# Kernel optimization log

Measured on AMD Instinct MI355X. Metric: run time of the kernel, lower is better.

## Reference

```python
import jax, jax.numpy as jnp
import numpy as np

HEADS = 8

def _flatten(x, s1, s2):
    # 'b c (h s1) (w s2) -> b (h w) (s1 s2 c)'
    b, c, H, W = x.shape
    h, w = H // s1, W // s2
    x = x.reshape(b, c, h, s1, w, s2).transpose(0, 2, 4, 3, 5, 1)
    return x.reshape(b, h * w, s1 * s2 * c)

def _unflatten(x, h, w, s1, s2):
    # 'b (h w) (s1 s2 c) -> b c (h s1) (w s2)'
    b, n, e = x.shape
    c = e // (s1 * s2)
    x = x.reshape(b, h, w, s1, s2, c).transpose(0, 5, 1, 3, 2, 4)
    return x.reshape(b, c, h * s1, w * s2)

def _attn(x_detail, x_context, wq, bq, wk, bk, wv, bv, wo, bo):
    E = x_detail.shape[-1]
    d = E // HEADS
    scale = d ** -0.5
    def split(t):
        b, n, _ = t.shape
        return t.reshape(b, n, HEADS, d).transpose(0, 2, 1, 3)  # b h n d
    q = split(x_context @ wq.T + bq)
    k = split(x_detail @ wk.T + bk)
    v = split(x_detail @ wv.T + bv)
    att = jax.nn.softmax(jnp.einsum('bhqd,bhkd->bhqk', q, k) * scale, axis=-1)
    out = jnp.einsum('bhqk,bhkd->bhqd', att, v)
    b, h, n, _ = out.shape
    out = out.transpose(0, 2, 1, 3).reshape(b, n, E)
    return out @ wo.T + bo

def setup_inputs() -> dict:
    key = jax.random.key(0)
    ks = iter(jax.random.split(key, 64))
    inp = {}
    xshapes = [(16, 96, 56, 56), (16, 192, 28, 28), (16, 384, 14, 14), (16, 768, 7, 7)]
    names = ['x00', 'x10', 'x20', 'x30']
    for nm, sh in zip(names, xshapes):
        inp[nm + '_detail'] = jax.random.normal(next(ks), sh, dtype=jnp.float32)
        inp[nm + '_context'] = jax.random.normal(next(ks), sh, dtype=jnp.float32)
    embs = [384, 192, 384, 768]
    for i, E in enumerate(embs):
        for p in ['q', 'k', 'v', 'o']:
            inp[f'w{p}{i}'] = jax.random.normal(next(ks), (E, E), dtype=jnp.float32) * 0.02
            inp[f'b{p}{i}'] = jnp.zeros((E,), dtype=jnp.float32)
    return inp

def reference(x00_detail, x00_context, x10_detail, x10_context,
              x20_detail, x20_context, x30_detail, x30_context,
              wq0, bq0, wk0, bk0, wv0, bv0, wo0, bo0,
              wq1, bq1, wk1, bk1, wv1, bv1, wo1, bo1,
              wq2, bq2, wk2, bk2, wv2, bv2, wo2, bo2,
              wq3, bq3, wk3, bk3, wv3, bv3, wo3, bo3):
    # scale 0: 56x56 with 2x2 patching -> 784 tokens, emb 384
    o0 = x00_detail + _unflatten(
        _attn(_flatten(x00_detail, 2, 2), _flatten(x00_context, 2, 2),
              wq0, bq0, wk0, bk0, wv0, bv0, wo0, bo0), 28, 28, 2, 2)
    # scale 1: 28x28 -> 784 tokens, emb 192
    o1 = x10_detail + _unflatten(
        _attn(_flatten(x10_detail, 1, 1), _flatten(x10_context, 1, 1),
              wq1, bq1, wk1, bk1, wv1, bv1, wo1, bo1), 28, 28, 1, 1)
    # scale 2: 14x14 -> 196 tokens, emb 384
    o2 = x20_detail + _unflatten(
        _attn(_flatten(x20_detail, 1, 1), _flatten(x20_context, 1, 1),
              wq2, bq2, wk2, bk2, wv2, bv2, wo2, bo2), 14, 14, 1, 1)
    # scale 3: 7x7 -> 49 tokens, emb 768
    o3 = x30_detail + _unflatten(
        _attn(_flatten(x30_detail, 1, 1), _flatten(x30_context, 1, 1),
              wq3, bq3, wk3, bk3, wv3, bv3, wo3, bo3), 7, 7, 1, 1)
    return (o0, o1, o2, o3)
```

## Files before the change

### kernel.cpp

```cpp
#include <hip/hip_runtime.h>
#include <hip/hip_bf16.h>
#include <cstdint>
#include <cstddef>
#include <cmath>

typedef unsigned short bf16u;
typedef float f32x4 __attribute__((ext_vector_type(4)));
typedef short frag8 __attribute__((ext_vector_type(8)));

typedef __attribute__((address_space(1))) uint32_t u32g;
typedef __attribute__((address_space(3))) uint32_t u32l;

__device__ __forceinline__ void async_cp16(const bf16u* g, bf16u* l) {
    __builtin_amdgcn_global_load_lds((u32g*)g, (u32l*)l, 16, 0, 0);
}

__device__ __forceinline__ bf16u f2bf(float f) {
    union { float f; uint32_t u; } v; v.f = f;
    uint32_t u = v.u;
    return (bf16u)((u + 0x7fffu + ((u >> 16) & 1u)) >> 16);
}

__device__ __forceinline__ uint32_t pk2bf(float a, float b) {
    __hip_bfloat162 h = __float22bfloat162_rn(make_float2(a, b));
    union { __hip_bfloat162 h; uint32_t u; } c; c.h = h; return c.u;
}

__device__ __forceinline__ int vperm(int n) {
    return (n & ~63) | ((n & 15) << 2) | ((n >> 4) & 3);
}

static constexpr int cN[4]   = {784, 784, 196, 49};
static constexpr int cE[4]   = {384, 192, 384, 768};
static constexpr int cM[4]   = {12544, 12544, 3136, 784};
static constexpr int cC[4]   = {96, 192, 384, 768};
static constexpr int cH[4]   = {56, 28, 14, 7};
static constexpr int cS[4]   = {2, 1, 1, 1};
static constexpr int cWt[4]  = {28, 28, 14, 7};

static constexpr size_t xoff[4] = {0, 4816896, 7225344, 8429568};
static constexpr size_t voff[4] = {0, 6815744, 10223616, 12320768};
static constexpr size_t woff[4] = {0, 589824, 737280, 1327104};

__device__ __constant__ float qsc[4] = {0.20823509f, 0.29448888f, 0.20823509f, 0.14724444f};

static constexpr int qStartQ[5] = {0, 294, 369, 411, 999};
static constexpr int oStart[5]  = {0,294,369,411,999};

static constexpr int fStart[9] = {0,4800,9600,12000,14400,15744,17088,17856,18624};
static constexpr int wCum[17]  = {0,72,144,216,288,306,324,342,360,432,504,576,648,936,1224,1512,1800};
static constexpr int fNtn[4] = {25, 25, 7, 2};
static constexpr int fNtc[4] = {3, 6, 12, 24};
static constexpr int fSp[4]  = {4, 1, 1, 1};

struct BiasP { const float* p[16]; };
struct PrepP { const float* x[8]; const float* w[16]; };
struct OunfP { const float* xd[4]; };

__global__ __launch_bounds__(256) void prep(PrepP pp, bf16u* __restrict__ Xd,
                                            bf16u* __restrict__ Xc, bf16u* __restrict__ Wb) {
    int blk = blockIdx.x, tid = threadIdx.x;
    if (blk < 18624) {
        __shared__ float tile[32][33];
        int seg = 0;
        while (seg < 7 && blk >= fStart[seg + 1]) seg++;
        int s = seg >> 1, which = seg & 1;
        int l = blk - fStart[seg];
        int ntn = fNtn[s], ntc = fNtc[s], sp = fSp[s];
        int nt = l % ntn; l /= ntn;
        int ctl = l % ntc; l /= ntc;
        int spi = l % sp; int b = l / sp;
        int sv = cS[s];
        int s1i = spi / sv, s2i = spi % sv;
        int C = cC[s], H = cH[s], Wd = cH[s], N = cN[s], E2 = cE[s], Wt = cWt[s];
        const float* x = pp.x[s * 2 + which];
        bf16u* dst = (which ? Xc : Xd) + xoff[s];
        int tx = tid & 31, ty = tid >> 5;
        int n0 = nt * 32, c0 = ctl * 32;
#pragma unroll
        for (int rr = 0; rr < 4; ++rr) {
            int c = c0 + rr * 8 + ty;
            int n = n0 + tx;
            if (n < N) {
                int hh = (n / Wt) * sv + s1i;
                int ww = (n % Wt) * sv + s2i;
                tile[rr * 8 + ty][tx] = x[((size_t)(b * C + c) * H + hh) * Wd + ww];
            }
        }
        __syncthreads();
        int ebase = (s1i * sv + s2i) * C + c0;
#pragma unroll
        for (int rr = 0; rr < 4; ++rr) {
            int n = n0 + rr * 8 + ty;
            if (n < N)
                dst[((size_t)b * N + n) * E2 + ebase + tx] = f2bf(tile[tx][rr * 8 + ty]);
        }
    } else {
        int wb = blk - 18624;
        int m2 = 0;
        while (m2 < 15 && wb >= wCum[m2 + 1]) m2++;
        int s = m2 >> 2, mi = m2 & 3;
        size_t e2 = (size_t)cE[s] * cE[s];
        size_t base = (size_t)(wb - wCum[m2]) * 2048 + tid * 8;
        const float* src = pp.w[m2];
        bf16u* dst = Wb + woff[s] + mi * e2 + base;
        float4 a = *(const float4*)(src + base);
        float4 c = *(const float4*)(src + base + 4);
        bf16u o[8] = {f2bf(a.x), f2bf(a.y), f2bf(a.z), f2bf(a.w),
                      f2bf(c.x), f2bf(c.y), f2bf(c.z), f2bf(c.w)};
        *(frag8*)dst = *(frag8*)o;
    }
}

template<int MODE, int NN, int DHt, int DHPt, int NJt>
__device__ __forceinline__ void gemm_tile128(const bf16u* __restrict__ A, const bf16u* __restrict__ W,
                                             const float* __restrict__ bias,
                                             int M, int E, int mTile, int eTile, float oscale,
                                             bf16u* __restrict__ outB,
                                             bf16u* sm) {
    bf16u* A0 = sm;
    bf16u* B0 = sm + 4096;
    bf16u* A1 = sm + 8192;
    bf16u* B1 = sm + 12288;
    int tid = threadIdx.x, wave = tid >> 6, lane = tid & 63;
    int mbase = mTile * 128, ebase = eTile * 128;
    int wm = (wave & 1) * 64, wn = (wave >> 1) * 64;
    f32x4 acc[4][4] = {};
    int srow = tid >> 2, sch = (tid & 3) * 8;
    int K = E;
    int m0 = mbase + srow;      if (m0 >= M) m0 = M - 1;
    int m1 = mbase + srow + 64; if (m1 >= M) m1 = M - 1;
    const bf16u* Ag0 = A + (size_t)m0 * K + sch;
    const bf16u* Ag1 = A + (size_t)m1 * K + sch;
    const bf16u* Wg0 = W + (size_t)(ebase + srow) * K + sch;
    const bf16u* Wg1 = W + (size_t)(ebase + srow + 64) * K + sch;
    int la = (lane & 15) * 32 + (lane >> 4) * 8;

    auto stage = [&](int k0, bf16u* As, bf16u* Bs) {
        async_cp16(Ag0 + k0, As + tid * 8);
        async_cp16(Ag1 + k0, As + 2048 + tid * 8);
        async_cp16(Wg0 + k0, Bs + tid * 8);
        async_cp16(Wg1 + k0, Bs + 2048 + tid * 8);
    };
    auto compute = [&](const bf16u* As, const bf16u* Bs) {
        frag8 af[4], bfr[4];
#pragma unroll
        for (int i = 0; i < 4; ++i) {
            af[i]  = *(const frag8*)(As + (wm + i * 16) * 32 + la);
            bfr[i] = *(const frag8*)(Bs + (wn + i * 16) * 32 + la);
        }
#pragma unroll
        for (int i = 0; i < 4; ++i)
#pragma unroll
            for (int j = 0; j < 4; ++j)
                acc[i][j] = __builtin_amdgcn_mfma_f32_16x16x32_bf16(af[i], bfr[j], acc[i][j], 0, 0, 0);
    };

    stage(0, A0, B0);
    __syncthreads();
    for (int k0 = 0; k0 < K; k0 += 64) {
        stage(k0 + 32, A1, B1);
        compute(A0, B0);
        __syncthreads();
        if (k0 + 64 < K) stage(k0 + 64, A0, B0);
        compute(A1, B1);
        if (k0 + 64 < K) __syncthreads();
    }

#pragma unroll
    for (int mt = 0; mt < 4; ++mt) {
#pragma unroll
        for (int nt = 0; nt < 4; ++nt) {
            int col = ebase + wn + nt * 16 + (lane & 15);
            float bv = bias[col];
            int rbase = mbase + wm + mt * 16 + (lane >> 4) * 4;
#pragma unroll
            for (int r = 0; r < 4; ++r) {
                int rowg = rbase + r;
                if (rowg >= M) continue;
                float val = (acc[mt][nt][r] + bv) * oscale;
                if (MODE == 0) {
                    outB[(size_t)rowg * E + col] = f2bf(val);
                } else {
                    int bb2 = rowg / NN, n = rowg % NN;
                    int hh = col / DHt, d = col - hh * DHt;
                    outB[((size_t)(bb2 * 8 + hh) * DHPt + d) * NJt + vperm(n)] = f2bf(val);
                }
            }
        }
    }
}

template<int MODE, int NN, int DHt, int DHPt, int NJt>
__device__ __forceinline__ void gemm_tile64(const bf16u* __restrict__ A, const bf16u* __restrict__ W,
                                            const float* __restrict__ bias,
                                            int M, int E, int mTile, int eTile, float oscale,
                                            bf16u* __restrict__ outB,
                                            bf16u* sm) {
    bf16u* A0 = sm;
    bf16u* B0 = sm + 2048;
    bf16u* A1 = sm + 4096;
    bf16u* B1 = sm + 6144;
    int tid = threadIdx.x, wave = tid >> 6, lane = tid & 63;
    int mbase = mTile * 64, ebase = eTile * 64;
    int wm = (wave & 1) * 32, wn = (wave >> 1) * 32;
    f32x4 acc[2][2] = {};
    int srow = tid >> 2, sch = (tid & 3) * 8;
    int K = E;
    int m = mbase + srow; if (m >= M) m = M - 1;
    const bf16u* Ag = A + (size_t)m * K + sch;
    const bf16u* Wg = W + (size_t)(ebase + srow) * K + sch;
    int la = (lane & 15) * 32 + (lane >> 4) * 8;

    auto stage = [&](int k0, bf16u* As, bf16u* Bs) {
        async_cp16(Ag + k0, As + tid * 8);
        async_cp16(Wg + k0, Bs + tid * 8);
    };
    auto compute = [&](const bf16u* As, const bf16u* Bs) {
        frag8 af0 = *(const frag8*)(As + wm * 32 + la);
        frag8 af1 = *(const frag8*)(As + (wm + 16) * 32 + la);
        frag8 bf0 = *(const frag8*)(Bs + wn * 32 + la);
        frag8 bf1 = *(const frag8*)(Bs + (wn + 16) * 32 + la);
        acc[0][0] = __builtin_amdgcn_mfma_f32_16x16x32_bf16(af0, bf0, acc[0][0], 0, 0, 0);
        acc[0][1] = __builtin_amdgcn_mfma_f32_16x16x32_bf16(af0, bf1, acc[0][1], 0, 0, 0);
        acc[1][0] = __builtin_amdgcn_mfma_f32_16x16x32_bf16(af1, bf0, acc[1][0], 0, 0, 0);
        acc[1][1] = __builtin_amdgcn_mfma_f32_16x16x32_bf16(af1, bf1, acc[1][1], 0, 0, 0);
    };

    stage(0, A0, B0);
    __syncthreads();
    for (int k0 = 0; k0 < K; k0 += 64) {
        stage(k0 + 32, A1, B1);
        compute(A0, B0);
        __syncthreads();
        if (k0 + 64 < K) stage(k0 + 64, A0, B0);
        compute(A1, B1);
        if (k0 + 64 < K) __syncthreads();
    }

#pragma unroll
    for (int mt = 0; mt < 2; ++mt) {
#pragma unroll
        for (int nt = 0; nt < 2; ++nt) {
            int col = ebase + wn + nt * 16 + (lane & 15);
            float bv = bias[col];
            int rbase = mbase + wm + mt * 16 + (lane >> 4) * 4;
#pragma unroll
            for (int r = 0; r < 4; ++r) {
                int rowg = rbase + r;
                if (rowg >= M) continue;
                float val = (acc[mt][nt][r] + bv) * oscale;
                if (MODE == 0) {
                    outB[(size_t)rowg * E + col] = f2bf(val);
                } else {
                    int bb2 = rowg / NN, n = rowg % NN;
                    int hh = col / DHt, d = col - hh * DHt;
                    outB[((size_t)(bb2 * 8 + hh) * DHPt + d) * NJt + vperm(n)] = f2bf(val);
                }
            }
        }
    }
}

template<int NN, int DHt, int DHPt, int NJt>
__device__ __forceinline__ void gemm_kv128(const bf16u* __restrict__ A, const bf16u* __restrict__ Wk,
                                           const bf16u* __restrict__ Wv,
                                           const float* __restrict__ bk, const float* __restrict__ bv,
                                           int M, int E, int mTile, int eTile,
                                           bf16u* __restrict__ Ko, bf16u* __restrict__ Vo, bf16u* sm) {
    bf16u* A0 = sm;           bf16u* K0 = sm + 4096;   bf16u* V0 = sm + 8192;
    bf16u* A1 = sm + 12288;   bf16u* K1 = sm + 16384;  bf16u* V1 = sm + 20480;
    int tid = threadIdx.x, wave = tid >> 6, lane = tid & 63;
    int mbase = mTile * 128, ebase = eTile * 128;
    int wm = (wave & 1) * 64, wn = (wave >> 1) * 64;
    f32x4 acck[4][4] = {};
    f32x4 accv[4][4] = {};
    int srow = tid >> 2, sch = (tid & 3) * 8;
    int Kd = E;
    int m0 = mbase + srow;      if (m0 >= M) m0 = M - 1;
    int m1 = mbase + srow + 64; if (m1 >= M) m1 = M - 1;
    const bf16u* Ag0 = A + (size_t)m0 * Kd + sch;
    const bf16u* Ag1 = A + (size_t)m1 * Kd + sch;
    const bf16u* Kg0 = Wk + (size_t)(ebase + srow) * Kd + sch;
    const bf16u* Kg1 = Wk + (size_t)(ebase + srow + 64) * Kd + sch;
    const bf16u* Vg0 = Wv + (size_t)(ebase + srow) * Kd + sch;
    const bf16u* Vg1 = Wv + (size_t)(ebase + srow + 64) * Kd + sch;
    int la = (lane & 15) * 32 + (lane >> 4) * 8;

    auto stage = [&](int k0, bf16u* As, bf16u* Ks, bf16u* Vs) {
        async_cp16(Ag0 + k0, As + tid * 8);
        async_cp16(Ag1 + k0, As + 2048 + tid * 8);
        async_cp16(Kg0 + k0, Ks + tid * 8);
        async_cp16(Kg1 + k0, Ks + 2048 + tid * 8);
        async_cp16(Vg0 + k0, Vs + tid * 8);
        async_cp16(Vg1 + k0, Vs + 2048 + tid * 8);
    };
    auto compute = [&](const bf16u* As, const bf16u* Ks, const bf16u* Vs) {
        frag8 af[4], bfr[4];
#pragma unroll
        for (int i = 0; i < 4; ++i)
            af[i] = *(const frag8*)(As + (wm + i * 16) * 32 + la);
#pragma unroll
        for (int i = 0; i < 4; ++i)
            bfr[i] = *(const frag8*)(Ks + (wn + i * 16) * 32 + la);
#pragma unroll
        for (int i = 0; i < 4; ++i)
#pragma unroll
            for (int j = 0; j < 4; ++j)
                acck[i][j] = __builtin_amdgcn_mfma_f32_16x16x32_bf16(af[i], bfr[j], acck[i][j], 0, 0, 0);
#pragma unroll
        for (int i = 0; i < 4; ++i)
            bfr[i] = *(const frag8*)(Vs + (wn + i * 16) * 32 + la);
#pragma unroll
        for (int i = 0; i < 4; ++i)
#pragma unroll
            for (int j = 0; j < 4; ++j)
                accv[i][j] = __builtin_amdgcn_mfma_f32_16x16x32_bf16(af[i], bfr[j], accv[i][j], 0, 0, 0);
    };

    stage(0, A0, K0, V0);
    __syncthreads();
    for (int k0 = 0; k0 < Kd; k0 += 64) {
        stage(k0 + 32, A1, K1, V1);
        compute(A0, K0, V0);
        __syncthreads();
        if (k0 + 64 < Kd) stage(k0 + 64, A0, K0, V0);
        compute(A1, K1, V1);
        if (k0 + 64 < Kd) __syncthreads();
    }

#pragma unroll
    for (int mt = 0; mt < 4; ++mt) {
#pragma unroll
        for (int nt = 0; nt < 4; ++nt) {
            int col = ebase + wn + nt * 16 + (lane & 15);
            float bkc = bk[col];
            float bvc = bv[col];
            int hh = col / DHt, d = col - hh * DHt;
            int rbase = mbase + wm + mt * 16 + (lane >> 4) * 4;
#pragma unroll
            for (int r = 0; r < 4; ++r) {
                int rowg = rbase + r;
                if (rowg >= M) continue;
                Ko[(size_t)rowg * E + col] = f2bf(acck[mt][nt][r] + bkc);
                int bb2 = rowg / NN, n = rowg % NN;
                Vo[((size_t)(bb2 * 8 + hh) * DHPt + d) * NJt + vperm(n)] = f2bf(accv[mt][nt][r] + bvc);
            }
        }
    }
}

template<int NN, int DHt, int DHPt, int NJt>
__device__ __forceinline__ void gemm_kv64(const bf16u* __restrict__ A, const bf16u* __restrict__ Wk,
                                          const bf16u* __restrict__ Wv,
                                          const float* __restrict__ bk, const float* __restrict__ bv,
                                          int M, int E, int mTile, int eTile,
                                          bf16u* __restrict__ Ko, bf16u* __restrict__ Vo, bf16u* sm) {
    bf16u* A0 = sm;          bf16u* K0 = sm + 2048;  bf16u* V0 = sm + 4096;
    bf16u* A1 = sm + 6144;   bf16u* K1 = sm + 8192;  bf16u* V1 = sm + 10240;
    int tid = threadIdx.x, wave = tid >> 6, lane = tid & 63;
    int mbase = mTile * 64, ebase = eTile * 64;
    int wm = (wave & 1) * 32, wn = (wave >> 1) * 32;
    f32x4 acck[2][2] = {};
    f32x4 accv[2][2] = {};
    int srow = tid >> 2, sch = (tid & 3) * 8;
    int Kd = E;
    int m = mbase + srow; if (m >= M) m = M - 1;
    const bf16u* Ag = A + (size_t)m * Kd + sch;
    const bf16u* Kg = Wk + (size_t)(ebase + srow) * Kd + sch;
    const bf16u* Vg = Wv + (size_t)(ebase + srow) * Kd + sch;
    int la = (lane & 15) * 32 + (lane >> 4) * 8;

    auto stage = [&](int k0, bf16u* As, bf16u* Ks, bf16u* Vs) {
        async_cp16(Ag + k0, As + tid * 8);
        async_cp16(Kg + k0, Ks + tid * 8);
        async_cp16(Vg + k0, Vs + tid * 8);
    };
    auto compute = [&](const bf16u* As, const bf16u* Ks, const bf16u* Vs) {
        frag8 af0 = *(const frag8*)(As + wm * 32 + la);
        frag8 af1 = *(const frag8*)(As + (wm + 16) * 32 + la);
        frag8 k0f = *(const frag8*)(Ks + wn * 32 + la);
        frag8 k1f = *(const frag8*)(Ks + (wn + 16) * 32 + la);
        acck[0][0] = __builtin_amdgcn_mfma_f32_16x16x32_bf16(af0, k0f, acck[0][0], 0, 0, 0);
        acck[0][1] = __builtin_amdgcn_mfma_f32_16x16x32_bf16(af0, k1f, acck[0][1], 0, 0, 0);
        acck[1][0] = __builtin_amdgcn_mfma_f32_16x16x32_bf16(af1, k0f, acck[1][0], 0, 0, 0);
        acck[1][1] = __builtin_amdgcn_mfma_f32_16x16x32_bf16(af1, k1f, acck[1][1], 0, 0, 0);
        frag8 v0f = *(const frag8*)(Vs + wn * 32 + la);
        frag8 v1f = *(const frag8*)(Vs + (wn + 16) * 32 + la);
        accv[0][0] = __builtin_amdgcn_mfma_f32_16x16x32_bf16(af0, v0f, accv[0][0], 0, 0, 0);
        accv[0][1] = __builtin_amdgcn_mfma_f32_16x16x32_bf16(af0, v1f, accv[0][1], 0, 0, 0);
        accv[1][0] = __builtin_amdgcn_mfma_f32_16x16x32_bf16(af1, v0f, accv[1][0], 0, 0, 0);
        accv[1][1] = __builtin_amdgcn_mfma_f32_16x16x32_bf16(af1, v1f, accv[1][1], 0, 0, 0);
    };

    stage(0, A0, K0, V0);
    __syncthreads();
    for (int k0 = 0; k0 < Kd; k0 += 64) {
        stage(k0 + 32, A1, K1, V1);
        compute(A0, K0, V0);
        __syncthreads();
        if (k0 + 64 < Kd) stage(k0 + 64, A0, K0, V0);
        compute(A1, K1, V1);
        if (k0 + 64 < Kd) __syncthreads();
    }

#pragma unroll
    for (int mt = 0; mt < 2; ++mt) {
#pragma unroll
        for (int nt = 0; nt < 2; ++nt) {
            int col = ebase + wn + nt * 16 + (lane & 15);
            float bkc = bk[col];
            float bvc = bv[col];
            int hh = col / DHt, d = col - hh * DHt;
            int rbase = mbase + wm + mt * 16 + (lane >> 4) * 4;
#pragma unroll
            for (int r = 0; r < 4; ++r) {
                int rowg = rbase + r;
                if (rowg >= M) continue;
                Ko[(size_t)rowg * E + col] = f2bf(acck[mt][nt][r] + bkc);
                int bb2 = rowg / NN, n = rowg % NN;
                Vo[((size_t)(bb2 * 8 + hh) * DHPt + d) * NJt + vperm(n)] = f2bf(accv[mt][nt][r] + bvc);
            }
        }
    }
}

__global__ __launch_bounds__(256) void qkv_q(const bf16u* __restrict__ Xc, const bf16u* __restrict__ Wb,
                                             bf16u* __restrict__ Qb, BiasP bp) {
    __shared__ __align__(16) bf16u sm[16384];
    int blk = blockIdx.x;
    int seg = 0;
    while (seg < 3 && blk >= qStartQ[seg + 1]) seg++;
    int t = blk - qStartQ[seg];
    if (seg < 3) {
        int s = (seg == 0) ? 0 : (seg == 1 ? 2 : 3);
        int E = cE[s], M = cM[s];
        int ct = E >> 7;
        int mTile = t / ct, eTile = t - mTile * ct;
        gemm_tile128<0, 0, 1, 0, 0>(Xc + xoff[s], Wb + woff[s], bp.p[s * 4], M, E, mTile, eTile,
                                    qsc[s], Qb + xoff[s], sm);
    } else {
        int E = 192, M = 12544;
        int mTile = t / 3, eTile = t - mTile * 3;
        gemm_tile64<0, 0, 1, 0, 0>(Xc + xoff[1], Wb + woff[1], bp.p[4], M, E, mTile, eTile,
                                   qsc[1], Qb + xoff[1], sm);
    }
}

__global__ __launch_bounds__(256, 2) void qkv_kv(const bf16u* __restrict__ Xd, const bf16u* __restrict__ Wb,
                                                 bf16u* __restrict__ Kb, bf16u* __restrict__ Vt, BiasP bp) {
    __shared__ __align__(16) bf16u sm[24576];
    int blk = blockIdx.x;
    int seg = 0;
    while (seg < 3 && blk >= qStartQ[seg + 1]) seg++;
    int t = blk - qStartQ[seg];
    if (seg < 3) {
        int s = (seg == 0) ? 0 : (seg == 1 ? 2 : 3);
        int E = cE[s], M = cM[s];
        int ct = E >> 7;
        int mTile = t / ct, eTile = t - mTile * ct;
        const bf16u* A  = Xd + xoff[s];
        const bf16u* Wk = Wb + woff[s] + (size_t)1 * E * E;
        const bf16u* Wv = Wb + woff[s] + (size_t)2 * E * E;
        if (s == 0)
            gemm_kv128<784, 48, 64, 832>(A, Wk, Wv, bp.p[1], bp.p[2], M, E, mTile, eTile,
                                         Kb + xoff[0], Vt + voff[0], sm);
        else if (s == 2)
            gemm_kv128<196, 48, 64, 256>(A, Wk, Wv, bp.p[9], bp.p[10], M, E, mTile, eTile,
                                         Kb + xoff[2], Vt + voff[2], sm);
        else
            gemm_kv128<49, 96, 96, 64>(A, Wk, Wv, bp.p[13], bp.p[14], M, E, mTile, eTile,
                                       Kb + xoff[3], Vt + voff[3], sm);
    } else {
        int E = 192, M = 12544;
        int mTile = t / 3, eTile = t - mTile * 3;
        gemm_kv64<784, 24, 32, 832>(Xd + xoff[1], Wb + woff[1] + (size_t)1 * E * E,
                                    Wb + woff[1] + (size_t)2 * E * E, bp.p[5], bp.p[6],
                                    M, E, mTile, eTile, Kb + xoff[1], Vt + voff[1], sm);
    }
}

__device__ __forceinline__ f32x4 bfly_add16(f32x4 v) {
#pragma unroll
    for (int m = 1; m <= 8; m <<= 1) {
        f32x4 o;
#pragma unroll
        for (int e = 0; e < 4; ++e) o[e] = __shfl_xor(v[e], m);
#pragma unroll
        for (int e = 0; e < 4; ++e) v[e] += o[e];
    }
    return v;
}

template<int DH, int N>
__device__ __forceinline__ void attn_body2(bf16u* __restrict__ smem,
                                           const bf16u* __restrict__ Q, const bf16u* __restrict__ K,
                                           const bf16u* __restrict__ Vt, bf16u* __restrict__ O,
                                           int lin) {
    constexpr int DHP = (DH == 24) ? 32 : 64;
    constexpr int C8  = DHP / 8;
    constexpr int CM  = C8 - 1;
    constexpr int KC  = DHP / 32;
    constexpr int DHT = (DH + 15) / 16;
    constexpr int VR  = DHT * 16;
    constexpr int NT  = (N + 63) / 64;
    constexpr int NJc = NT * 64;
    constexpr int E   = DH * 8;
    constexpr int KS  = 64 * C8;
    constexpr int TS  = KS + VR * 8;
    constexpr int RND = (TS + 255) / 256;
    constexpr int PP  = 72;

    bf16u* buf0 = smem;
    bf16u* buf1 = smem + (size_t)TS * 8;
    bf16u* Ps   = smem + (size_t)2 * TS * 8;

    const int qt = lin % NT;
    const int r2 = lin / NT;
    const int h = r2 & 7, b = r2 >> 3;
    const int qb = qt * 64;
    const int tid = threadIdx.x, wave = tid >> 6, lane = tid & 63;
    const int mrow = lane & 15, quad = lane >> 4;

    const bf16u* Kb2 = K + (size_t)b * N * E + h * DH;
    const bf16u* Vb2 = Vt + (size_t)(b * 8 + h) * DHP * NJc;

    auto stage = [&](int jt, bf16u* buf) {
#pragma unroll
        for (int r = 0; r < RND; ++r) {
            int s = tid + r * 256;
            bf16u* dst = buf + (size_t)s * 8;
            if (s < KS) {
                int row = s / C8;
                int cl = (s & CM) ^ (row & CM);
                int n = jt * 64 + row; if (n >= N) n = N - 1;
                async_cp16(Kb2 + (size_t)n * E + cl * 8, dst);
            } else if (s < TS) {
                int v = s - KS;
                int d = v >> 3;
                int cl = (v & 7) ^ (d & 7);
                async_cp16(Vb2 + (size_t)d * NJc + jt * 64 + cl * 8, dst);
            }
        }
    };

    stage(0, buf0);

    frag8 qf[KC];
    {
        int qn = qb + wave * 16 + mrow; if (qn >= N) qn = N - 1;
        const bf16u* qp = Q + (size_t)(b * N + qn) * E + h * DH;
#pragma unroll
        for (int kc = 0; kc < KC; ++kc) {
            int col = kc * 32 + quad * 8;
            frag8 v = {};
            if (col < DH) v = *(const frag8*)(qp + col);
            qf[kc] = v;
        }
    }

    f32x4 lrun = {0.f, 0.f, 0.f, 0.f};
    f32x4 oacc[DHT];
#pragma unroll
    for (int t = 0; t < DHT; ++t) oacc[t] = f32x4{0.f, 0.f, 0.f, 0.f};

    bf16u* Pw = Ps + wave * 16 * PP;

    __syncthreads();

    int p = 0;
    for (int jt = 0; jt < NT; ++jt) {
        bf16u* KsB = p ? buf1 : buf0;
        bf16u* VsB = KsB + (size_t)KS * 8;
        if (jt + 1 < NT) stage(jt + 1, p ? buf0 : buf1);

        f32x4 s[4];
        const bool domask = ((N & 63) != 0) && (jt == NT - 1);
#pragma unroll
        for (int sub = 0; sub < 4; ++sub) {
            f32x4 acc = {};
#pragma unroll
            for (int kc = 0; kc < KC; ++kc) {
                int c = kc * 4 + quad;
                frag8 bfr = *(const frag8*)(KsB + ((size_t)((sub * 16 + mrow) * C8 + (c ^ (mrow & CM)))) * 8);
                acc = __builtin_amdgcn_mfma_f32_16x16x32_bf16(qf[kc], bfr, acc, 0, 0, 0);
            }
            if (domask) {
                int col = jt * 64 + sub * 16 + mrow;
                if (col >= N) { acc[0] = acc[1] = acc[2] = acc[3] = -30000.f; }
            }
            s[sub] = acc;
        }

#pragma unroll
        for (int sub = 0; sub < 4; ++sub)
#pragma unroll
            for (int e = 0; e < 4; ++e) {
                float px = __builtin_amdgcn_exp2f(s[sub][e]);
                s[sub][e] = px;
                lrun[e] += px;
            }

#pragma unroll
        for (int e = 0; e < 4; ++e) {
            uint2 u;
            u.x = pk2bf(s[0][e], s[1][e]);
            u.y = pk2bf(s[2][e], s[3][e]);
            *(uint2*)(Pw + (quad * 4 + e) * PP + mrow * 4) = u;
        }

#pragma unroll
        for (int jc = 0; jc < 2; ++jc) {
            frag8 af = *(const frag8*)(Pw + mrow * PP + jc * 32 + quad * 8);
            int c = jc * 4 + quad;
#pragma unroll
            for (int t = 0; t < DHT; ++t) {
                frag8 bfr = *(const frag8*)(VsB + ((size_t)((t * 16 + mrow) * 8 + (c ^ (mrow & 7)))) * 8);
                oacc[t] = __builtin_amdgcn_mfma_f32_16x16x32_bf16(af, bfr, oacc[t], 0, 0, 0);
            }
        }
        __syncthreads();
        p ^= 1;
    }

    lrun = bfly_add16(lrun);
    f32x4 linv;
#pragma unroll
    for (int e = 0; e < 4; ++e) linv[e] = 1.0f / lrun[e];
#pragma unroll
    for (int t = 0; t < DHT; ++t) {
        int d = t * 16 + mrow;
        if (d >= DH) continue;
#pragma unroll
        for (int e = 0; e < 4; ++e) {
            int n = qb + wave * 16 + quad * 4 + e;
            if (n < N)
                O[((size_t)(b * N + n)) * E + h * DH + d] = f2bf(oacc[t][e] * linv[e]);
        }
    }
}

__global__ __launch_bounds__(256, 4) void attn_fat(const bf16u* __restrict__ Qb, const bf16u* __restrict__ Kb,
                                                   const bf16u* __restrict__ Vt, bf16u* __restrict__ Ob) {
    __shared__ __align__(16) bf16u smem[18944];
    int g = blockIdx.x;
    if (g < 1664) {
        int l = (g & 7) * 208 + (g >> 3);
        attn_body2<48, 784>(smem, Qb + xoff[0], Kb + xoff[0], Vt + voff[0], Ob + xoff[0], l);
    } else if (g < 3328) {
        int gg = g - 1664;
        int l = (gg & 7) * 208 + (gg >> 3);
        attn_body2<24, 784>(smem, Qb + xoff[1], Kb + xoff[1], Vt + voff[1], Ob + xoff[1], l);
    } else {
        int gg = g - 3328;
        int l = (gg & 7) * 64 + (gg >> 3);
        attn_body2<48, 196>(smem, Qb + xoff[2], Kb + xoff[2], Vt + voff[2], Ob + xoff[2], l);
    }
}

__global__ __launch_bounds__(256, 2) void attn_s3(const bf16u* __restrict__ Qg, const bf16u* __restrict__ Kg,
                                                  const bf16u* __restrict__ Vtg, bf16u* __restrict__ Og) {
    constexpr int DH = 96, N = 49, DHP = 96, KC = 3, DHT = 6, NJc = 64, E = 768;
    constexpr int KP = 104, QP = 104, VP = 72, PP = 72, C8 = 12;
    __shared__ __align__(16) bf16u smem[20224];
    bf16u* Ks = smem;
    bf16u* Vs = Ks + 64 * KP;
    bf16u* QsPw = Vs + DHT * 16 * VP;

    const bf16u* Q = Qg + xoff[3];
    const bf16u* K = Kg + xoff[3];
    const bf16u* Vt = Vtg + voff[3];
    bf16u* O = Og + xoff[3];

    int lin = blockIdx.x;
    int h = lin & 7, b = lin >> 3;
    int tid = threadIdx.x, wave = tid >> 6, lane = tid & 63;
    int mrow = lane & 15, quad = lane >> 4;

    for (int idx = tid; idx < 64 * C8; idx += 256) {
        int row = idx / C8, col = (idx % C8) * 8;
        int n = row; if (n >= N) n = N - 1;
        frag8 v = {};
        if (col < DH) v = *(const frag8*)(Q + ((size_t)(b * N + n)) * E + h * DH + col);
        *(frag8*)(QsPw + row * QP + col) = v;
    }
    for (int idx = tid; idx < 64 * C8; idx += 256) {
        int row = idx / C8, col = (idx % C8) * 8;
        int n = row; if (n >= N) n = N - 1;
        frag8 v = {};
        if (col < DH) v = *(const frag8*)(K + (size_t)(b * N + n) * E + h * DH + col);
        *(frag8*)(Ks + row * KP + col) = v;
    }
    const bf16u* Vb2 = Vt + (size_t)(b * 8 + h) * DHP * NJc;
    for (int idx = tid; idx < DHT * 16 * 8; idx += 256) {
        int d = idx / 8, j = (idx % 8) * 8;
        frag8 v = {};
        if (d < DH) v = *(const frag8*)(Vb2 + (size_t)d * NJc + j);
        *(frag8*)(Vs + d * VP + j) = v;
    }
    __syncthreads();
    frag8 qf[KC];
#pragma unroll
    for (int kc = 0; kc < KC; ++kc)
        qf[kc] = *(const frag8*)(QsPw + (wave * 16 + mrow) * QP + kc * 32 + quad * 8);
    __syncthreads();
    bf16u* Pw = QsPw + wave * 16 * PP;

    f32x4 lrun = {0.f, 0.f, 0.f, 0.f};
    f32x4 oacc[DHT];
#pragma unroll
    for (int t = 0; t < DHT; ++t) oacc[t] = f32x4{0.f, 0.f, 0.f, 0.f};

    f32x4 s[4];
#pragma unroll
    for (int sub = 0; sub < 4; ++sub) {
        f32x4 acc = {};
#pragma unroll
        for (int kc = 0; kc < KC; ++kc) {
            frag8 bfr = *(const frag8*)(Ks + (sub * 16 + mrow) * KP + kc * 32 + quad * 8);
            acc = __builtin_amdgcn_mfma_f32_16x16x32_bf16(qf[kc], bfr, acc, 0, 0, 0);
        }
        int col = sub * 16 + mrow;
        if (col >= N) { acc[0] = acc[1] = acc[2] = acc[3] = -30000.f; }
        s[sub] = acc;
    }
#pragma unroll
    for (int sub = 0; sub < 4; ++sub)
#pragma unroll
        for (int e = 0; e < 4; ++e) {
            float px = __builtin_amdgcn_exp2f(s[sub][e]);
            s[sub][e] = px;
            lrun[e] += px;
        }
#pragma unroll
    for (int e = 0; e < 4; ++e) {
        uint2 u;
        u.x = pk2bf(s[0][e], s[1][e]);
        u.y = pk2bf(s[2][e], s[3][e]);
        *(uint2*)(Pw + (quad * 4 + e) * PP + mrow * 4) = u;
    }
#pragma unroll
    for (int jc = 0; jc < 2; ++jc) {
        frag8 af = *(const frag8*)(Pw + mrow * PP + jc * 32 + quad * 8);
#pragma unroll
        for (int t = 0; t < DHT; ++t) {
            frag8 bfr = *(const frag8*)(Vs + (t * 16 + mrow) * VP + jc * 32 + quad * 8);
            oacc[t] = __builtin_amdgcn_mfma_f32_16x16x32_bf16(af, bfr, oacc[t], 0, 0, 0);
        }
    }

    lrun = bfly_add16(lrun);
    f32x4 linv;
#pragma unroll
    for (int e = 0; e < 4; ++e) linv[e] = 1.0f / lrun[e];
#pragma unroll
    for (int t = 0; t < DHT; ++t) {
        int d = t * 16 + mrow;
#pragma unroll
        for (int e = 0; e < 4; ++e) {
            int n = wave * 16 + quad * 4 + e;
            if (n < N)
                O[((size_t)(b * N + n)) * E + h * DH + d] = f2bf(oacc[t][e] * linv[e]);
        }
    }
}

template<int SC>
__device__ __forceinline__ size_t out_index(int rowg, int cg) {
    if (SC == 0) {
        int b = rowg / 784, n = rowg - b * 784;
        int slot = cg / 96, c = cg - slot * 96;
        int hh = n / 28, ww = n - hh * 28;
        return ((size_t)(b * 96 + c) * 56 + 2 * hh + (slot >> 1)) * 56 + 2 * ww + (slot & 1);
    } else if (SC == 1) {
        int b = rowg / 784, n = rowg - b * 784;
        return ((size_t)(b * 192 + cg)) * 784 + n;
    } else if (SC == 2) {
        int b = rowg / 196, n = rowg - b * 196;
        return ((size_t)(b * 384 + cg)) * 196 + n;
    } else {
        int b = rowg / 49, n = rowg - b * 49;
        return ((size_t)(b * 768 + cg)) * 49 + n;
    }
}

template<int SC>
__device__ __forceinline__ void o_tile128(const bf16u* __restrict__ A, const bf16u* __restrict__ W,
                                          const float* __restrict__ bias,
                                          const float* __restrict__ xd, float* __restrict__ out,
                                          int M, int E, int mTile, int eTile, bf16u* sm) {
    bf16u* A0 = sm;
    bf16u* B0 = sm + 4096;
    bf16u* A1 = sm + 8192;
    bf16u* B1 = sm + 12288;
    int tid = threadIdx.x, wave = tid >> 6, lane = tid & 63;
    int mbase = mTile * 128, ebase = eTile * 128;
    int wm = (wave & 1) * 64, wn = (wave >> 1) * 64;
    int mrow = lane & 15, quad = lane >> 4;
    f32x4 acc[4][4] = {};
    int srow = tid >> 2, sch = (tid & 3) * 8;
    int K = E;
    int m0 = mbase + srow;      if (m0 >= M) m0 = M - 1;
    int m1 = mbase + srow + 64; if (m1 >= M) m1 = M - 1;
    const bf16u* Ag0 = A + (size_t)m0 * K + sch;
    const bf16u* Ag1 = A + (size_t)m1 * K + sch;
    const bf16u* Wg0 = W + (size_t)(ebase + srow) * K + sch;
    const bf16u* Wg1 = W + (size_t)(ebase + srow + 64) * K + sch;
    int la = mrow * 32 + quad * 8;

    auto stage = [&](int k0, bf16u* As, bf16u* Bs) {
        async_cp16(Ag0 + k0, As + tid * 8);
        async_cp16(Ag1 + k0, As + 2048 + tid * 8);
        async_cp16(Wg0 + k0, Bs + tid * 8);
        async_cp16(Wg1 + k0, Bs + 2048 + tid * 8);
    };
    auto compute = [&](const bf16u* As, const bf16u* Bs) {
        frag8 af[4], bfr[4];
#pragma unroll
        for (int i = 0; i < 4; ++i) {
            af[i]  = *(const frag8*)(As + (wm + i * 16) * 32 + la);
            bfr[i] = *(const frag8*)(Bs + (wn + i * 16) * 32 + la);
        }
#pragma unroll
        for (int i = 0; i < 4; ++i)
#pragma unroll
            for (int j = 0; j < 4; ++j)
                acc[i][j] = __builtin_amdgcn_mfma_f32_16x16x32_bf16(af[i], bfr[j], acc[i][j], 0, 0, 0);
    };

    stage(0, A0, B0);
    __syncthreads();
    for (int k0 = 0; k0 < K; k0 += 64) {
        stage(k0 + 32, A1, B1);
        compute(A0, B0);
        __syncthreads();
        if (k0 + 64 < K) stage(k0 + 64, A0, B0);
        compute(A1, B1);
        if (k0 + 64 < K) __syncthreads();
    }

    float* Ls = (float*)sm;
#pragma unroll
    for (int ph = 0; ph < 4; ++ph) {
        __syncthreads();
        if ((wave & 1) == (ph >> 1)) {
            int mt0 = (ph & 1) * 2;
#pragma unroll
            for (int mi = 0; mi < 2; ++mi) {
                int mt = mt0 + mi;
#pragma unroll
                for (int nt = 0; nt < 4; ++nt)
#pragma unroll
                    for (int r = 0; r < 4; ++r)
                        Ls[(mi * 16 + quad * 4 + r) * 133 + wn + nt * 16 + mrow] = acc[mt][nt][r];
            }
        }
        __syncthreads();
        int rb = mbase + ph * 32;
#pragma unroll
        for (int i = 0; i < 16; ++i) {
            int coll = (tid >> 5) + i * 8;
            int l = tid & 31;
            int rg = rb + l;
            if (rg < M) {
                int cg = ebase + coll;
                size_t oi = out_index<SC>(rg, cg);
                out[oi] = xd[oi] + Ls[l * 133 + coll] + bias[cg];
            }
        }
    }
}

__device__ __forceinline__ void o_tile64_s1(const bf16u* __restrict__ A, const bf16u* __restrict__ W,
                                            const float* __restrict__ bias,
                                            const float* __restrict__ xd, float* __restrict__ out,
                                            int M, int E, int mTile, int eTile, bf16u* sm) {
    bf16u* A0 = sm;
    bf16u* B0 = sm + 2048;
    bf16u* A1 = sm + 4096;
    bf16u* B1 = sm + 6144;
    int tid = threadIdx.x, wave = tid >> 6, lane = tid & 63;
    int mbase = mTile * 64, ebase = eTile * 64;
    int wm = (wave & 1) * 32, wn = (wave >> 1) * 32;
    int mrow = lane & 15, quad = lane >> 4;
    f32x4 acc[2][2] = {};
    int srow = tid >> 2, sch = (tid & 3) * 8;
    int K = E;
    int m = mbase + srow; if (m >= M) m = M - 1;
    const bf16u* Ag = A + (size_t)m * K + sch;
    const bf16u* Wg = W + (size_t)(ebase + srow) * K + sch;
    int la = mrow * 32 + quad * 8;

    auto stage = [&](int k0, bf16u* As, bf16u* Bs) {
        async_cp16(Ag + k0, As + tid * 8);
        async_cp16(Wg + k0, Bs + tid * 8);
    };
    auto compute = [&](const bf16u* As, const bf16u* Bs) {
        frag8 af0 = *(const frag8*)(As + wm * 32 + la);
        frag8 af1 = *(const frag8*)(As + (wm + 16) * 32 + la);
        frag8 bf0 = *(const frag8*)(Bs + wn * 32 + la);
        frag8 bf1 = *(const frag8*)(Bs + (wn + 16) * 32 + la);
        acc[0][0] = __builtin_amdgcn_mfma_f32_16x16x32_bf16(af0, bf0, acc[0][0], 0, 0, 0);
        acc[0][1] = __builtin_amdgcn_mfma_f32_16x16x32_bf16(af0, bf1, acc[0][1], 0, 0, 0);
        acc[1][0] = __builtin_amdgcn_mfma_f32_16x16x32_bf16(af1, bf0, acc[1][0], 0, 0, 0);
        acc[1][1] = __builtin_amdgcn_mfma_f32_16x16x32_bf16(af1, bf1, acc[1][1], 0, 0, 0);
    };

    stage(0, A0, B0);
    __syncthreads();
    for (int k0 = 0; k0 < K; k0 += 64) {
        stage(k0 + 32, A1, B1);
        compute(A0, B0);
        __syncthreads();
        if (k0 + 64 < K) stage(k0 + 64, A0, B0);
        compute(A1, B1);
        if (k0 + 64 < K) __syncthreads();
    }

    float* Ls = (float*)sm;
#pragma unroll
    for (int ph = 0; ph < 2; ++ph) {
        __syncthreads();
        if ((wave & 1) == ph) {
#pragma unroll
            for (int mt = 0; mt < 2; ++mt)
#pragma unroll
                for (int nt = 0; nt < 2; ++nt)
#pragma unroll
                    for (int r = 0; r < 4; ++r)
                        Ls[(mt * 16 + quad * 4 + r) * 69 + wn + nt * 16 + mrow] = acc[mt][nt][r];
        }
        __syncthreads();
        int rb = mbase + ph * 32;
#pragma unroll
        for (int i = 0; i < 8; ++i) {
            int coll = (tid >> 5) + i * 8;
            int l = tid & 31;
            int rg = rb + l;
            if (rg < M) {
                int cg = ebase + coll;
                size_t oi = out_index<1>(rg, cg);
                out[oi] = xd[oi] + Ls[l * 69 + coll] + bias[cg];
            }
        }
    }
}

__global__ __launch_bounds__(256) void ounf_fat(const bf16u* __restrict__ Ob, const bf16u* __restrict__ Wb,
                                                float* __restrict__ out, BiasP bp, OunfP up) {
    __shared__ __align__(16) bf16u sm[16384];
    int blk = blockIdx.x;
    int seg = 0;
    while (seg < 3 && blk >= oStart[seg + 1]) seg++;
    int t = blk - oStart[seg];
    if (seg < 3) {
        int s = (seg == 0) ? 0 : (seg == 1 ? 2 : 3);
        int E = cE[s], M = cM[s];
        int ct = E >> 7;
        int mTile = t / ct, eTile = t - mTile * ct;
        const bf16u* A = Ob + xoff[s];
        const bf16u* W = Wb + woff[s] + (size_t)3 * E * E;
        if (s == 0)
            o_tile128<0>(A, W, bp.p[3], up.xd[0], out + xoff[0], M, E, mTile, eTile, sm);
        else if (s == 2)
            o_tile128<2>(A, W, bp.p[11], up.xd[2], out + xoff[2], M, E, mTile, eTile, sm);
        else
            o_tile128<3>(A, W, bp.p[15], up.xd[3], out + xoff[3], M, E, mTile, eTile, sm);
    } else {
        int E = 192, M = 12544;
        int mTile = t / 3, eTile = t - mTile * 3;
        o_tile64_s1(Ob + xoff[1], Wb + woff[1] + (size_t)3 * E * E, bp.p[7],
                    up.xd[1], out + xoff[1], M, E, mTile, eTile, sm);
    }
}

extern "C" void kernel_launch(void* const* d_in, const int* in_sizes, int n_in,
                              void* d_out, int out_size, void* d_ws, size_t ws_size,
                              hipStream_t stream) {
    bf16u* ws = (bf16u*)d_ws;
    bf16u* Qb = ws;
    bf16u* Kb = ws + 9031680;
    bf16u* Vt = ws + 18063360;
    bf16u* Ob = ws + 31170560;
    bf16u* Wb = ws + 40202240;
    bf16u* Xd = ws + 43888640;
    bf16u* Xc = ws + 52920320;
    float* out = (float*)d_out;

    PrepP pp; BiasP bb; OunfP ux;
    for (int s = 0; s < 4; ++s) {
        pp.x[s * 2]     = (const float*)d_in[s * 2];
        pp.x[s * 2 + 1] = (const float*)d_in[s * 2 + 1];
        ux.xd[s]        = (const float*)d_in[s * 2];
        int w0 = 8 + s * 8;
        pp.w[s * 4 + 0] = (const float*)d_in[w0 + 0];
        pp.w[s * 4 + 1] = (const float*)d_in[w0 + 2];
        pp.w[s * 4 + 2] = (const float*)d_in[w0 + 4];
        pp.w[s * 4 + 3] = (const float*)d_in[w0 + 6];
        bb.p[s * 4 + 0] = (const float*)d_in[w0 + 1];
        bb.p[s * 4 + 1] = (const float*)d_in[w0 + 3];
        bb.p[s * 4 + 2] = (const float*)d_in[w0 + 5];
        bb.p[s * 4 + 3] = (const float*)d_in[w0 + 7];
    }

    prep<<<20424, 256, 0, stream>>>(pp, Xd, Xc, Wb);
    qkv_q<<<999, 256, 0, stream>>>(Xc, Wb, Qb, bb);
    qkv_kv<<<999, 256, 0, stream>>>(Xd, Wb, Kb, Vt, bb);
    attn_fat<<<3840, 256, 0, stream>>>(Qb, Kb, Vt, Ob);
    attn_s3<<<128, 256, 0, stream>>>(Qb, Kb, Vt, Ob);
    ounf_fat<<<999, 256, 0, stream>>>(Ob, Wb, out, bb, ux);
}
```

Measured before the change: 379.1 us.

## Process 128 queries per attention block so each K/V tile is reused twice

The attention kernel for scales 0-2 now gives each wave 32 query rows (two 16-row MFMA tiles) instead of 16, so every block covers 128 queries and each staged K/V tile in LDS feeds twice as many MFMAs. This halves the number of blocks and the total K/V global-to-LDS traffic. In exchange it doubles accumulator registers and enlarges the P buffer in shared memory, and lowers the launch-bounds occupancy target from 4 to 3 blocks. The grid shrinks from 3840 to 2048 blocks, and the 196-token scale now has a mostly padded second query tile.

```diff
diff --git a/kernel.cpp b/kernel.cpp
--- a/kernel.cpp
+++ b/kernel.cpp
@@ -493,7 +493,7 @@
 }
 
 template<int DH, int N>
-__device__ __forceinline__ void attn_body2(bf16u* __restrict__ smem,
+__device__ __forceinline__ void attn_body3(bf16u* __restrict__ smem,
                                            const bf16u* __restrict__ Q, const bf16u* __restrict__ K,
                                            const bf16u* __restrict__ Vt, bf16u* __restrict__ O,
                                            int lin) {
@@ -504,6 +504,7 @@
     constexpr int DHT = (DH + 15) / 16;
     constexpr int VR  = DHT * 16;
     constexpr int NT  = (N + 63) / 64;
+    constexpr int QT  = (N + 127) / 128;
     constexpr int NJc = NT * 64;
     constexpr int E   = DH * 8;
     constexpr int KS  = 64 * C8;
@@ -515,10 +516,10 @@
     bf16u* buf1 = smem + (size_t)TS * 8;
     bf16u* Ps   = smem + (size_t)2 * TS * 8;
 
-    const int qt = lin % NT;
-    const int r2 = lin / NT;
+    const int qt = lin % QT;
+    const int r2 = lin / QT;
     const int h = r2 & 7, b = r2 >> 3;
-    const int qb = qt * 64;
+    const int qb = qt * 128;
     const int tid = threadIdx.x, wave = tid >> 6, lane = tid & 63;
     const int mrow = lane & 15, quad = lane >> 4;
 
@@ -546,25 +547,28 @@
 
     stage(0, buf0);
 
-    frag8 qf[KC];
+    frag8 qf0[KC], qf1[KC];
     {
-        int qn = qb + wave * 16 + mrow; if (qn >= N) qn = N - 1;
-        const bf16u* qp = Q + (size_t)(b * N + qn) * E + h * DH;
+        int qn0 = qb + wave * 32 + mrow;      if (qn0 >= N) qn0 = N - 1;
+        int qn1 = qb + wave * 32 + 16 + mrow; if (qn1 >= N) qn1 = N - 1;
+        const bf16u* qp0 = Q + (size_t)(b * N + qn0) * E + h * DH;
+        const bf16u* qp1 = Q + (size_t)(b * N + qn1) * E + h * DH;
 #pragma unroll
         for (int kc = 0; kc < KC; ++kc) {
             int col = kc * 32 + quad * 8;
-            frag8 v = {};
-            if (col < DH) v = *(const frag8*)(qp + col);
-            qf[kc] = v;
-        }
-    }
-
-    f32x4 lrun = {0.f, 0.f, 0.f, 0.f};
-    f32x4 oacc[DHT];
-#pragma unroll
-    for (int t = 0; t < DHT; ++t) oacc[t] = f32x4{0.f, 0.f, 0.f, 0.f};
-
-    bf16u* Pw = Ps + wave * 16 * PP;
+            frag8 v0 = {}, v1 = {};
+            if (col < DH) { v0 = *(const frag8*)(qp0 + col); v1 = *(const frag8*)(qp1 + col); }
+            qf0[kc] = v0; qf1[kc] = v1;
+        }
+    }
+
+    f32x4 lrun0 = {0.f, 0.f, 0.f, 0.f};
+    f32x4 lrun1 = {0.f, 0.f, 0.f, 0.f};
+    f32x4 oacc0[DHT], oacc1[DHT];
+#pragma unroll
+    for (int t = 0; t < DHT; ++t) { oacc0[t] = f32x4{0.f,0.f,0.f,0.f}; oacc1[t] = f32x4{0.f,0.f,0.f,0.f}; }
+
+    bf16u* Pw = Ps + wave * 32 * PP;
 
     __syncthreads();
 
@@ -574,87 +578,101 @@
         bf16u* VsB = KsB + (size_t)KS * 8;
         if (jt + 1 < NT) stage(jt + 1, p ? buf0 : buf1);
 
-        f32x4 s[4];
+        f32x4 s0[4], s1[4];
         const bool domask = ((N & 63) != 0) && (jt == NT - 1);
 #pragma unroll
         for (int sub = 0; sub < 4; ++sub) {
-            f32x4 acc = {};
+            f32x4 a0 = {}, a1 = {};
 #pragma unroll
             for (int kc = 0; kc < KC; ++kc) {
                 int c = kc * 4 + quad;
                 frag8 bfr = *(const frag8*)(KsB + ((size_t)((sub * 16 + mrow) * C8 + (c ^ (mrow & CM)))) * 8);
-                acc = __builtin_amdgcn_mfma_f32_16x16x32_bf16(qf[kc], bfr, acc, 0, 0, 0);
+                a0 = __builtin_amdgcn_mfma_f32_16x16x32_bf16(qf0[kc], bfr, a0, 0, 0, 0);
+                a1 = __builtin_amdgcn_mfma_f32_16x16x32_bf16(qf1[kc], bfr, a1, 0, 0, 0);
             }
             if (domask) {
                 int col = jt * 64 + sub * 16 + mrow;
-                if (col >= N) { acc[0] = acc[1] = acc[2] = acc[3] = -30000.f; }
-            }
-            s[sub] = acc;
+                if (col >= N) {
+                    a0[0] = a0[1] = a0[2] = a0[3] = -30000.f;
+                    a1[0] = a1[1] = a1[2] = a1[3] = -30000.f;
+                }
+            }
+            s0[sub] = a0; s1[sub] = a1;
         }
 
 #pragma unroll
         for (int sub = 0; sub < 4; ++sub)
 #pragma unroll
             for (int e = 0; e < 4; ++e) {
-                float px = __builtin_amdgcn_exp2f(s[sub][e]);
-                s[sub][e] = px;
-                lrun[e] += px;
+                float p0 = __builtin_amdgcn_exp2f(s0[sub][e]);
+                float p1 = __builtin_amdgcn_exp2f(s1[sub][e]);
+                s0[sub][e] = p0; s1[sub][e] = p1;
+                lrun0[e] += p0; lrun1[e] += p1;
             }
 
 #pragma unroll
         for (int e = 0; e < 4; ++e) {
-            uint2 u;
-            u.x = pk2bf(s[0][e], s[1][e]);
-            u.y = pk2bf(s[2][e], s[3][e]);
-            *(uint2*)(Pw + (quad * 4 + e) * PP + mrow * 4) = u;
+            uint2 u0, u1;
+            u0.x = pk2bf(s0[0][e], s0[1][e]);
+            u0.y = pk2bf(s0[2][e], s0[3][e]);
+            u1.x = pk2bf(s1[0][e], s1[1][e]);
+            u1.y = pk2bf(s1[2][e], s1[3][e]);
+            *(uint2*)(Pw + (quad * 4 + e) * PP + mrow * 4) = u0;
+            *(uint2*)(Pw + (16 + quad * 4 + e) * PP + mrow * 4) = u1;
         }
 
 #pragma unroll
         for (int jc = 0; jc < 2; ++jc) {
-            frag8 af = *(const frag8*)(Pw + mrow * PP + jc * 32 + quad * 8);
+            frag8 af0 = *(const frag8*)(Pw + mrow * PP + jc * 32 + quad * 8);
+            frag8 af1 = *(const frag8*)(Pw + (16 + mrow) * PP + jc * 32 + quad * 8);
             int c = jc * 4 + quad;
 #pragma unroll
             for (int t = 0; t < DHT; ++t) {
                 frag8 bfr = *(const frag8*)(VsB + ((size_t)((t * 16 + mrow) * 8 + (c ^ (mrow & 7)))) * 8);
-                oacc[t] = __builtin_amdgcn_mfma_f32_16x16x32_bf16(af, bfr, oacc[t], 0, 0, 0);
+                oacc0[t] = __builtin_amdgcn_mfma_f32_16x16x32_bf16(af0, bfr, oacc0[t], 0, 0, 0);
+                oacc1[t] = __builtin_amdgcn_mfma_f32_16x16x32_bf16(af1, bfr, oacc1[t], 0, 0, 0);
             }
         }
         __syncthreads();
         p ^= 1;
     }
 
-    lrun = bfly_add16(lrun);
-    f32x4 linv;
-#pragma unroll
-    for (int e = 0; e < 4; ++e) linv[e] = 1.0f / lrun[e];
+    lrun0 = bfly_add16(lrun0);
+    lrun1 = bfly_add16(lrun1);
+    f32x4 linv0, linv1;
+#pragma unroll
+    for (int e = 0; e < 4; ++e) { linv0[e] = 1.0f / lrun0[e]; linv1[e] = 1.0f / lrun1[e]; }
 #pragma unroll
     for (int t = 0; t < DHT; ++t) {
         int d = t * 16 + mrow;
         if (d >= DH) continue;
 #pragma unroll
         for (int e = 0; e < 4; ++e) {
-            int n = qb + wave * 16 + quad * 4 + e;
-            if (n < N)
-                O[((size_t)(b * N + n)) * E + h * DH + d] = f2bf(oacc[t][e] * linv[e]);
-        }
-    }
-}
-
-__global__ __launch_bounds__(256, 4) void attn_fat(const bf16u* __restrict__ Qb, const bf16u* __restrict__ Kb,
+            int n0 = qb + wave * 32 + quad * 4 + e;
+            int n1 = n0 + 16;
+            if (n0 < N)
+                O[((size_t)(b * N + n0)) * E + h * DH + d] = f2bf(oacc0[t][e] * linv0[e]);
+            if (n1 < N)
+                O[((size_t)(b * N + n1)) * E + h * DH + d] = f2bf(oacc1[t][e] * linv1[e]);
+        }
+    }
+}
+
+__global__ __launch_bounds__(256, 3) void attn_fat(const bf16u* __restrict__ Qb, const bf16u* __restrict__ Kb,
                                                    const bf16u* __restrict__ Vt, bf16u* __restrict__ Ob) {
-    __shared__ __align__(16) bf16u smem[18944];
+    __shared__ __align__(16) bf16u smem[23552];
     int g = blockIdx.x;
-    if (g < 1664) {
-        int l = (g & 7) * 208 + (g >> 3);
-        attn_body2<48, 784>(smem, Qb + xoff[0], Kb + xoff[0], Vt + voff[0], Ob + xoff[0], l);
-    } else if (g < 3328) {
-        int gg = g - 1664;
-        int l = (gg & 7) * 208 + (gg >> 3);
-        attn_body2<24, 784>(smem, Qb + xoff[1], Kb + xoff[1], Vt + voff[1], Ob + xoff[1], l);
+    if (g < 896) {
+        int l = (g & 7) * 112 + (g >> 3);
+        attn_body3<48, 784>(smem, Qb + xoff[0], Kb + xoff[0], Vt + voff[0], Ob + xoff[0], l);
+    } else if (g < 1792) {
+        int gg = g - 896;
+        int l = (gg & 7) * 112 + (gg >> 3);
+        attn_body3<24, 784>(smem, Qb + xoff[1], Kb + xoff[1], Vt + voff[1], Ob + xoff[1], l);
     } else {
-        int gg = g - 3328;
-        int l = (gg & 7) * 64 + (gg >> 3);
-        attn_body2<48, 196>(smem, Qb + xoff[2], Kb + xoff[2], Vt + voff[2], Ob + xoff[2], l);
+        int gg = g - 1792;
+        int l = (gg & 7) * 32 + (gg >> 3);
+        attn_body3<48, 196>(smem, Qb + xoff[2], Kb + xoff[2], Vt + voff[2], Ob + xoff[2], l);
     }
 }
 
@@ -1006,7 +1024,7 @@
     prep<<<20424, 256, 0, stream>>>(pp, Xd, Xc, Wb);
     qkv_q<<<999, 256, 0, stream>>>(Xc, Wb, Qb, bb);
     qkv_kv<<<999, 256, 0, stream>>>(Xd, Wb, Kb, Vt, bb);
-    attn_fat<<<3840, 256, 0, stream>>>(Qb, Kb, Vt, Ob);
+    attn_fat<<<2048, 256, 0, stream>>>(Qb, Kb, Vt, Ob);
     attn_s3<<<128, 256, 0, stream>>>(Qb, Kb, Vt, Ob);
     ounf_fat<<<999, 256, 0, stream>>>(Ob, Wb, out, bb, ux);
 }
```

Measured after the change: 376.1 us. Within noise of the previous version (-0.8%).
